# Kernel tuning notes

Measured on AMD Instinct MI355X. Metric: run time of the kernel, lower is better.

Reference implementation:

```python
import jax, jax.numpy as jnp
import numpy as np

DIM = 1024
HEADS = 16
HEAD_DIM = DIM // HEADS
HIDDEN = 4 * DIM
EPS = 1e-6


def _layer_norm(x, scale, bias):
    mu = jnp.mean(x, axis=-1, keepdims=True)
    var = jnp.mean(jnp.square(x - mu), axis=-1, keepdims=True)
    return (x - mu) * jax.lax.rsqrt(var + EPS) * scale + bias


def setup_inputs() -> dict:
    key = jax.random.key(0)
    ks = jax.random.split(key, 8)
    s = 0.02
    return {
        "x": jax.random.normal(ks[0], (8, 1024, DIM), dtype=jnp.float32),
        "w_qkv": jax.random.normal(ks[1], (DIM, 3 * DIM), dtype=jnp.float32) * s,
        "b_qkv": jnp.zeros((3 * DIM,), jnp.float32),
        "w_proj": jax.random.normal(ks[2], (DIM, DIM), dtype=jnp.float32) * s,
        "b_proj": jnp.zeros((DIM,), jnp.float32),
        "ln1_scale": jnp.ones((DIM,), jnp.float32),
        "ln1_bias": jnp.zeros((DIM,), jnp.float32),
        "ln2_scale": jnp.ones((DIM,), jnp.float32),
        "ln2_bias": jnp.zeros((DIM,), jnp.float32),
        "w_fc1": jax.random.normal(ks[3], (DIM, HIDDEN), dtype=jnp.float32) * s,
        "b_fc1": jnp.zeros((HIDDEN,), jnp.float32),
        "w_fc2": jax.random.normal(ks[4], (HIDDEN, DIM), dtype=jnp.float32) * s,
        "b_fc2": jnp.zeros((DIM,), jnp.float32),
    }


def reference(x, w_qkv, b_qkv, w_proj, b_proj, ln1_scale, ln1_bias,
              ln2_scale, ln2_bias, w_fc1, b_fc1, w_fc2, b_fc2):
    B, N, C = x.shape
    scale = HEAD_DIM ** -0.5

    # --- attention branch ---
    h = _layer_norm(x, ln1_scale, ln1_bias)
    qkv = h @ w_qkv + b_qkv                          # [B,N,3C]
    qkv = qkv.reshape(B, N, 3, HEADS, HEAD_DIM)
    qkv = jnp.transpose(qkv, (2, 0, 3, 1, 4))        # [3,B,H,N,D]
    q, k, v = qkv[0], qkv[1], qkv[2]
    attn = jnp.einsum("bhnd,bhmd->bhnm", q, k) * scale
    attn = jax.nn.softmax(attn, axis=-1)
    o = jnp.einsum("bhnm,bhmd->bhnd", attn, v)       # [B,H,N,D]
    o = jnp.transpose(o, (0, 2, 1, 3)).reshape(B, N, C)
    x = x + (o @ w_proj + b_proj)

    # --- mlp branch ---
    h = _layer_norm(x, ln2_scale, ln2_bias)
    h = jax.nn.gelu(h @ w_fc1 + b_fc1)               # tanh approx, matches flax default
    x = x + (h @ w_fc2 + b_fc2)
    return x
```

## Files before the change

### kernel.cpp

```cpp
#include <hip/hip_runtime.h>

typedef __attribute__((ext_vector_type(8))) short short8;
typedef __attribute__((ext_vector_type(4))) float f32x4;
typedef unsigned short ushort;
typedef unsigned int uint;

#define DIM 1024
#define NSEQ 1024
#define BATCH 8
#define HEADS 16
#define HD 64
#define HIDDEN 4096
#define NROWS (BATCH * NSEQ)

__device__ inline ushort f2bf(float f) {
  uint u = __float_as_uint(f);
  u += 0x7fff + ((u >> 16) & 1);
  return (ushort)(u >> 16);
}

__device__ inline f32x4 zero4() {
  f32x4 z; z[0] = 0.f; z[1] = 0.f; z[2] = 0.f; z[3] = 0.f; return z;
}

__device__ inline float gelu_fast(float x) {
  float u2 = 1.5957691216057308f * (x + 0.044715f * x * x * x);
  float e = __builtin_amdgcn_exp2f(-1.4426950408889634f * u2);
  return x / (1.0f + e);
}

#define GLDS16(g, l)                                                  \
  __builtin_amdgcn_global_load_lds(                                   \
      (const __attribute__((address_space(1))) void*)(g),             \
      (__attribute__((address_space(3))) void*)(l), 16, 0, 0)

#define WAITVM(n) asm volatile("s_waitcnt vmcnt(" #n ")" ::: "memory")

__global__ __launch_bounds__(256) void ln_kernel(
    const float* __restrict__ x, const float* __restrict__ sc,
    const float* __restrict__ bi, ushort* __restrict__ out) {
  int row = blockIdx.x;
  int t = threadIdx.x;
  const float4 v = reinterpret_cast<const float4*>(x + (size_t)row * DIM)[t];
  float s = v.x + v.y + v.z + v.w;
  float s2 = v.x * v.x + v.y * v.y + v.z * v.z + v.w * v.w;
#pragma unroll
  for (int off = 32; off >= 1; off >>= 1) {
    s += __shfl_xor(s, off);
    s2 += __shfl_xor(s2, off);
  }
  __shared__ float ps[4], ps2[4];
  int w = t >> 6;
  if ((t & 63) == 0) { ps[w] = s; ps2[w] = s2; }
  __syncthreads();
  s = ps[0] + ps[1] + ps[2] + ps[3];
  s2 = ps2[0] + ps2[1] + ps2[2] + ps2[3];
  float mu = s * (1.0f / DIM);
  float var = s2 * (1.0f / DIM) - mu * mu;
  float rstd = rsqrtf(var + 1e-6f);
  float4 scv = reinterpret_cast<const float4*>(sc)[t];
  float4 biv = reinterpret_cast<const float4*>(bi)[t];
  ushort4 o;
  o.x = f2bf((v.x - mu) * rstd * scv.x + biv.x);
  o.y = f2bf((v.y - mu) * rstd * scv.y + biv.y);
  o.z = f2bf((v.z - mu) * rstd * scv.z + biv.z);
  o.w = f2bf((v.w - mu) * rstd * scv.w + biv.w);
  reinterpret_cast<ushort4*>(out + (size_t)row * DIM)[t] = o;
}

__global__ __launch_bounds__(256) void wtrans_kernel(
    const float* __restrict__ w, ushort* __restrict__ wt, int K, int N) {
  __shared__ float tile[32][33];
  int n0 = blockIdx.x * 32, k0 = blockIdx.y * 32;
  int tx = threadIdx.x & 31, ty = threadIdx.x >> 5;
#pragma unroll
  for (int j = 0; j < 4; j++)
    tile[ty + 8 * j][tx] = w[(size_t)(k0 + ty + 8 * j) * N + n0 + tx];
  __syncthreads();
#pragma unroll
  for (int j = 0; j < 4; j++)
    wt[(size_t)(n0 + ty + 8 * j) * K + k0 + tx] = f2bf(tile[tx][ty + 8 * j]);
}

__global__ __launch_bounds__(256) void vtrans_kernel(
    const ushort* __restrict__ qkv, ushort* __restrict__ vT) {
  __shared__ ushort Ts[64 * 64];
  int bh = blockIdx.y;
  int b = bh >> 4, h = bh & 15;
  int n0 = blockIdx.x * 64;
  int t = threadIdx.x;
  const ushort* src = qkv + (size_t)b * NSEQ * 3072 + 2048 + h * 64;
#pragma unroll
  for (int i = 0; i < 2; i++) {
    int ci = i * 256 + t;
    int rr = ci >> 3, c = ci & 7;
    short8 v = *reinterpret_cast<const short8*>(src + (size_t)(n0 + rr) * 3072 + c * 8);
    *reinterpret_cast<short8*>(&Ts[rr * 64 + ((c ^ (rr >> 3)) & 7) * 8]) = v;
  }
  __syncthreads();
  ushort* dst = vT + (size_t)bh * 64 * NSEQ;
#pragma unroll
  for (int i = 0; i < 2; i++) {
    int ci = i * 256 + t;
    int dd = ci >> 3, c = ci & 7;
    short8 v;
#pragma unroll
    for (int j = 0; j < 8; j++) {
      int nn = c * 8 + j;
      v[j] = (short)Ts[nn * 64 + (((dd >> 3) ^ (nn >> 3)) & 7) * 8 + (dd & 7)];
    }
    *reinterpret_cast<short8*>(dst + (size_t)dd * NSEQ + n0 + c * 8) = v;
  }
}

template <int BN, int EPI>
__global__ __launch_bounds__(512, 2) void gemm256_kernel(
    const ushort* __restrict__ A, const ushort* __restrict__ Bt,
    const float* __restrict__ bias, const float* __restrict__ res,
    void* __restrict__ outp, int M, int N, int K) {
  constexpr int BM = 256, BK = 32;
  constexpr int WM = (BN == 256) ? 2 : 4;
  constexpr int WN = 8 / WM;
  constexpr int MR = (BM / WM) / 16;
  constexpr int NR = (BN / WN) / 16;
  constexpr int PH = MR / 4;
  constexpr int AR = 2;
  constexpr int BR = BN / 128;
  static_assert(BN == 256 || BN == 128, "");

  __shared__ ushort As[4][BM * BK];
  __shared__ ushort Bs[4][BN * BK];

  int t = threadIdx.x, lane = t & 63, w = t >> 6;
  int wr = w / WN, wc = w % WN;
  int r = lane & 15, g = lane >> 4;

  int nwg = gridDim.x * gridDim.y;
  int flat = blockIdx.y * gridDim.x + blockIdx.x;
  int swzf = (flat & 7) * (nwg >> 3) + (flat >> 3);
  int bx = swzf % gridDim.x, by = swzf / gridDim.x;
  int m0 = by * BM, n0 = bx * BN;

  const ushort* Ab = A + (size_t)m0 * K;
  const ushort* Bb = Bt + (size_t)n0 * K;

  int srow = t >> 2;
  int sgc8 = (((t & 3) ^ (srow & 3) ^ ((srow >> 2) & 3)) & 3) * 8;
  int swb = (w << 4) * BK;
  int sw = ((g ^ (r & 3) ^ ((r >> 2) & 3)) & 3) * 8;

  auto stageA = [&](int kt2) {
    ushort* as = &As[kt2 & 3][0];
    int ko = kt2 * BK;
#pragma unroll
    for (int p = 0; p < AR; p++)
      GLDS16(Ab + (size_t)(p * 128 + srow) * K + ko + sgc8,
             as + p * 128 * BK + swb);
  };
  auto stageB = [&](int kt2) {
    ushort* bs = &Bs[kt2 & 3][0];
    int ko = kt2 * BK;
#pragma unroll
    for (int p = 0; p < BR; p++)
      GLDS16(Bb + (size_t)(p * 128 + srow) * K + ko + sgc8,
             bs + p * 128 * BK + swb);
  };

  f32x4 acc[MR][NR];
#pragma unroll
  for (int mi = 0; mi < MR; mi++)
#pragma unroll
    for (int ni = 0; ni < NR; ni++) acc[mi][ni] = zero4();

  int nkt = K / BK;

  stageA(0); stageB(0);
  stageA(1); stageB(1);
  stageA(2); stageB(2);
  if constexpr (BN == 256) WAITVM(8); else WAITVM(6);
  __builtin_amdgcn_s_barrier();
  asm volatile("" ::: "memory");

  for (int kt = 0; kt < nkt; kt++) {
    const ushort* as = &As[kt & 3][0];
    const ushort* bs = &Bs[kt & 3][0];
    short8 b[NR];
#pragma unroll
    for (int ph = 0; ph < PH; ph++) {
      if (ph == 0) {
#pragma unroll
        for (int ni = 0; ni < NR; ni++)
          b[ni] = *reinterpret_cast<const short8*>(
              &bs[(wc * (BN / WN) + ni * 16 + r) * BK + sw]);
      }
      short8 a[4];
#pragma unroll
      for (int i = 0; i < 4; i++)
        a[i] = *reinterpret_cast<const short8*>(
            &as[(wr * (BM / WM) + (ph * 4 + i) * 16 + r) * BK + sw]);
      if (kt + 3 < nkt) {
        if constexpr (PH == 2) {
          if (ph == 0) stageA(kt + 3); else stageB(kt + 3);
        } else {
          stageA(kt + 3); stageB(kt + 3);
        }
      }
      if (ph == PH - 1) {
        if (kt + 3 < nkt) {
          if constexpr (BN == 256) WAITVM(8); else WAITVM(6);
        } else if (kt + 2 < nkt) {
          if constexpr (BN == 256) WAITVM(4); else WAITVM(3);
        } else if (kt + 1 < nkt) {
          WAITVM(0);
        }
      }
      __builtin_amdgcn_s_barrier();
      asm volatile("s_waitcnt lgkmcnt(0)" ::: "memory");
      __builtin_amdgcn_sched_barrier(0);
      __builtin_amdgcn_s_setprio(1);
#pragma unroll
      for (int i = 0; i < 4; i++)
#pragma unroll
        for (int ni = 0; ni < NR; ni++)
          acc[ph * 4 + i][ni] = __builtin_amdgcn_mfma_f32_16x16x32_bf16(
              a[i], b[ni], acc[ph * 4 + i][ni], 0, 0, 0);
      __builtin_amdgcn_s_setprio(0);
      __builtin_amdgcn_s_barrier();
      asm volatile("" ::: "memory");
    }
  }

  int rg = g * 4;
#pragma unroll
  for (int mi = 0; mi < MR; mi++) {
#pragma unroll
    for (int ni = 0; ni < NR; ni++) {
      int row = m0 + wr * (BM / WM) + mi * 16 + rg;
      int col = n0 + wc * (BN / WN) + ni * 16 + r;
      float bv = bias[col];
#pragma unroll
      for (int j = 0; j < 4; j++) {
        float v = acc[mi][ni][j] + bv;
        if (EPI == 1) v = gelu_fast(v);
        if (EPI == 2) {
          reinterpret_cast<float*>(outp)[(size_t)(row + j) * N + col] =
              v + res[(size_t)(row + j) * N + col];
        } else {
          reinterpret_cast<ushort*>(outp)[(size_t)(row + j) * N + col] = f2bf(v);
        }
      }
    }
  }
}

#define SM_SCALE_L2E 0.18033688f
#define SM_BIAS_L2E 11.54156036f
__global__ __launch_bounds__(256) void attn_kernel(
    const ushort* __restrict__ qkv, const ushort* __restrict__ vT,
    ushort* __restrict__ o) {
  __shared__ ushort Kt[64 * 72];
  __shared__ ushort Vt[64 * 72];
  __shared__ ushort Pl[4][16 * 72];
  int q0 = blockIdx.x * 64, h = blockIdx.y, b = blockIdx.z;
  int t = threadIdx.x, lane = t & 63, w = t >> 6;
  int r = lane & 15, g = lane >> 4;
  const ushort* base = qkv + (size_t)b * NSEQ * 3072 + h * 64;
  const ushort* vbase = vT + (size_t)(b * HEADS + h) * 64 * NSEQ;

  short8 qf[2];
  {
    const ushort* qrow = base + (size_t)(q0 + w * 16 + r) * 3072;
    qf[0] = *reinterpret_cast<const short8*>(qrow + g * 8);
    qf[1] = *reinterpret_cast<const short8*>(qrow + 32 + g * 8);
  }

  float l[4] = {0.f, 0.f, 0.f, 0.f};
  f32x4 oacc[4];
#pragma unroll
  for (int db = 0; db < 4; db++) oacc[db] = zero4();

  int srw = t >> 3, sc8 = (t & 7) * 8;
  for (int kt = 0; kt < NSEQ / 64; kt++) {
    int k0 = kt * 64;
    short8 kreg[2], vreg[2];
#pragma unroll
    for (int i = 0; i < 2; i++) {
      int rw = srw + i * 32;
      kreg[i] = *reinterpret_cast<const short8*>(base + 1024 + (size_t)(k0 + rw) * 3072 + sc8);
      vreg[i] = *reinterpret_cast<const short8*>(vbase + (size_t)rw * NSEQ + k0 + sc8);
    }
    __syncthreads();
#pragma unroll
    for (int i = 0; i < 2; i++) {
      int rw = srw + i * 32;
      *reinterpret_cast<short8*>(&Kt[rw * 72 + sc8]) = kreg[i];
      *reinterpret_cast<short8*>(&Vt[rw * 72 + sc8]) = vreg[i];
    }
    __syncthreads();

#pragma unroll
    for (int kb = 0; kb < 4; kb++) {
      short8 kf0 = *reinterpret_cast<const short8*>(&Kt[(kb * 16 + r) * 72 + g * 8]);
      short8 kf1 = *reinterpret_cast<const short8*>(&Kt[(kb * 16 + r) * 72 + 32 + g * 8]);
      f32x4 z = zero4();
      z = __builtin_amdgcn_mfma_f32_16x16x32_bf16(qf[0], kf0, z, 0, 0, 0);
      z = __builtin_amdgcn_mfma_f32_16x16x32_bf16(qf[1], kf1, z, 0, 0, 0);
#pragma unroll
      for (int j = 0; j < 4; j++) {
        float p = __builtin_amdgcn_exp2f(fmaf(z[j], SM_SCALE_L2E, -SM_BIAS_L2E));
        l[j] += p;
        Pl[w][(g * 4 + j) * 72 + kb * 16 + r] = (ushort)(__float_as_uint(p) >> 16);
      }
    }

#pragma unroll
    for (int ks = 0; ks < 2; ks++) {
      short8 pa = *reinterpret_cast<const short8*>(&Pl[w][r * 72 + ks * 32 + g * 8]);
#pragma unroll
      for (int db = 0; db < 4; db++) {
        short8 vb = *reinterpret_cast<const short8*>(&Vt[(db * 16 + r) * 72 + ks * 32 + g * 8]);
        oacc[db] = __builtin_amdgcn_mfma_f32_16x16x32_bf16(pa, vb, oacc[db], 0, 0, 0);
      }
    }
  }

#pragma unroll
  for (int j = 0; j < 4; j++) {
#pragma unroll
    for (int off = 8; off >= 1; off >>= 1) l[j] += __shfl_xor(l[j], off);
    l[j] = 1.0f / l[j];
  }

#pragma unroll
  for (int db = 0; db < 4; db++)
#pragma unroll
    for (int j = 0; j < 4; j++) {
      size_t row = (size_t)b * NSEQ + q0 + w * 16 + g * 4 + j;
      int col = h * 64 + db * 16 + r;
      o[row * DIM + col] = f2bf(oacc[db][j] * l[j]);
    }
}

extern "C" void kernel_launch(void* const* d_in, const int* in_sizes, int n_in,
                              void* d_out, int out_size, void* d_ws, size_t ws_size,
                              hipStream_t stream) {
  const float* x      = (const float*)d_in[0];
  const float* w_qkv  = (const float*)d_in[1];
  const float* b_qkv  = (const float*)d_in[2];
  const float* w_proj = (const float*)d_in[3];
  const float* b_proj = (const float*)d_in[4];
  const float* ln1s   = (const float*)d_in[5];
  const float* ln1b   = (const float*)d_in[6];
  const float* ln2s   = (const float*)d_in[7];
  const float* ln2b   = (const float*)d_in[8];
  const float* w_fc1  = (const float*)d_in[9];
  const float* b_fc1  = (const float*)d_in[10];
  const float* w_fc2  = (const float*)d_in[11];
  const float* b_fc2  = (const float*)d_in[12];
  float* out = (float*)d_out;

  char* ws = (char*)d_ws;
  ushort* wqkv_t  = (ushort*)(ws);
  ushort* wproj_t = (ushort*)(ws + 6291456);
  ushort* wfc1_t  = (ushort*)(ws + 8388608);
  ushort* wfc2_t  = (ushort*)(ws + 16777216);
  ushort* hbuf    = (ushort*)(ws + 25165824);
  float*  x1      = (float*)(ws + 41943040);
  ushort* vTb     = (ushort*)(ws + 41943040);
  ushort* qkv     = (ushort*)(ws + 75497472);
  ushort* obuf    = (ushort*)(ws + 125829120);
  ushort* fc1a    = qkv;

  wtrans_kernel<<<dim3(3072 / 32, 1024 / 32), 256, 0, stream>>>(w_qkv, wqkv_t, 1024, 3072);
  wtrans_kernel<<<dim3(1024 / 32, 1024 / 32), 256, 0, stream>>>(w_proj, wproj_t, 1024, 1024);
  wtrans_kernel<<<dim3(4096 / 32, 1024 / 32), 256, 0, stream>>>(w_fc1, wfc1_t, 1024, 4096);
  wtrans_kernel<<<dim3(1024 / 32, 4096 / 32), 256, 0, stream>>>(w_fc2, wfc2_t, 4096, 1024);

  ln_kernel<<<NROWS, 256, 0, stream>>>(x, ln1s, ln1b, hbuf);
  gemm256_kernel<128, 0><<<dim3(3072 / 128, NROWS / 256), 512, 0, stream>>>(
      hbuf, wqkv_t, b_qkv, nullptr, qkv, NROWS, 3072, 1024);
  vtrans_kernel<<<dim3(NSEQ / 64, BATCH * HEADS), 256, 0, stream>>>(qkv, vTb);
  attn_kernel<<<dim3(NSEQ / 64, HEADS, BATCH), 256, 0, stream>>>(qkv, vTb, obuf);
  gemm256_kernel<128, 2><<<dim3(1024 / 128, NROWS / 256), 512, 0, stream>>>(
      obuf, wproj_t, b_proj, x, x1, NROWS, 1024, 1024);

  ln_kernel<<<NROWS, 256, 0, stream>>>(x1, ln2s, ln2b, hbuf);
  gemm256_kernel<256, 1><<<dim3(4096 / 256, NROWS / 256), 512, 0, stream>>>(
      hbuf, wfc1_t, b_fc1, nullptr, fc1a, NROWS, 4096, 1024);
  gemm256_kernel<128, 2><<<dim3(1024 / 128, NROWS / 256), 512, 0, stream>>>(
      fc1a, wfc2_t, b_fc2, x1, out, NROWS, 1024, 4096);
}
```

Before: 398.8 us.

## Software-pipeline GEMM with register double-buffered fragments and one barrier per k-tile

Restructures the GEMM main loop so the LDS fragments for the next k-tile are loaded into a second register set while the MFMAs for the current tile run. A and B are staged together three tiles ahead, and there is now one barrier per k-tile instead of several per phase. K becomes a template constant so loop bounds and address strides are known at compile time. The aim is to hide LDS read latency and cut synchronisation overhead, at the cost of more VGPRs and a tighter dependence on ds_read completion ordering around the barrier.

```diff
diff --git a/kernel.cpp b/kernel.cpp
--- a/kernel.cpp
+++ b/kernel.cpp
@@ -35,6 +35,7 @@
       (__attribute__((address_space(3))) void*)(l), 16, 0, 0)
 
 #define WAITVM(n) asm volatile("s_waitcnt vmcnt(" #n ")" ::: "memory")
+#define SBAR() asm volatile("s_barrier" ::: "memory")
 
 __global__ __launch_bounds__(256) void ln_kernel(
     const float* __restrict__ x, const float* __restrict__ sc,
@@ -113,20 +114,21 @@
   }
 }
 
-template <int BN, int EPI>
+template <int BN, int EPI, int KK>
 __global__ __launch_bounds__(512, 2) void gemm256_kernel(
     const ushort* __restrict__ A, const ushort* __restrict__ Bt,
     const float* __restrict__ bias, const float* __restrict__ res,
-    void* __restrict__ outp, int M, int N, int K) {
+    void* __restrict__ outp, int M, int N) {
   constexpr int BM = 256, BK = 32;
   constexpr int WM = (BN == 256) ? 2 : 4;
   constexpr int WN = 8 / WM;
   constexpr int MR = (BM / WM) / 16;
   constexpr int NR = (BN / WN) / 16;
-  constexpr int PH = MR / 4;
   constexpr int AR = 2;
   constexpr int BR = BN / 128;
+  constexpr int nkt = KK / BK;
   static_assert(BN == 256 || BN == 128, "");
+  static_assert(nkt >= 4 && (nkt % 2) == 0, "");
 
   __shared__ ushort As[4][BM * BK];
   __shared__ ushort Bs[4][BN * BK];
@@ -141,93 +143,78 @@
   int bx = swzf % gridDim.x, by = swzf / gridDim.x;
   int m0 = by * BM, n0 = bx * BN;
 
-  const ushort* Ab = A + (size_t)m0 * K;
-  const ushort* Bb = Bt + (size_t)n0 * K;
+  const ushort* Ab = A + (size_t)m0 * KK;
+  const ushort* Bb = Bt + (size_t)n0 * KK;
 
   int srow = t >> 2;
   int sgc8 = (((t & 3) ^ (srow & 3) ^ ((srow >> 2) & 3)) & 3) * 8;
   int swb = (w << 4) * BK;
   int sw = ((g ^ (r & 3) ^ ((r >> 2) & 3)) & 3) * 8;
 
-  auto stageA = [&](int kt2) {
+  auto stageAB = [&](int kt2) {
     ushort* as = &As[kt2 & 3][0];
-    int ko = kt2 * BK;
-#pragma unroll
-    for (int p = 0; p < AR; p++)
-      GLDS16(Ab + (size_t)(p * 128 + srow) * K + ko + sgc8,
-             as + p * 128 * BK + swb);
-  };
-  auto stageB = [&](int kt2) {
     ushort* bs = &Bs[kt2 & 3][0];
     int ko = kt2 * BK;
 #pragma unroll
+    for (int p = 0; p < AR; p++)
+      GLDS16(Ab + (size_t)(p * 128 + srow) * KK + ko + sgc8,
+             as + p * 128 * BK + swb);
+#pragma unroll
     for (int p = 0; p < BR; p++)
-      GLDS16(Bb + (size_t)(p * 128 + srow) * K + ko + sgc8,
+      GLDS16(Bb + (size_t)(p * 128 + srow) * KK + ko + sgc8,
              bs + p * 128 * BK + swb);
   };
 
+  auto ldfrags = [&](int kt2, short8 (&fa_)[MR], short8 (&fb_)[NR]) {
+    const ushort* as = &As[kt2 & 3][0];
+    const ushort* bs = &Bs[kt2 & 3][0];
+#pragma unroll
+    for (int mi = 0; mi < MR; mi++)
+      fa_[mi] = *reinterpret_cast<const short8*>(
+          &as[(wr * (BM / WM) + mi * 16 + r) * BK + sw]);
+#pragma unroll
+    for (int ni = 0; ni < NR; ni++)
+      fb_[ni] = *reinterpret_cast<const short8*>(
+          &bs[(wc * (BN / WN) + ni * 16 + r) * BK + sw]);
+  };
+
   f32x4 acc[MR][NR];
 #pragma unroll
   for (int mi = 0; mi < MR; mi++)
 #pragma unroll
     for (int ni = 0; ni < NR; ni++) acc[mi][ni] = zero4();
 
-  int nkt = K / BK;
-
-  stageA(0); stageB(0);
-  stageA(1); stageB(1);
-  stageA(2); stageB(2);
-  if constexpr (BN == 256) WAITVM(8); else WAITVM(6);
-  __builtin_amdgcn_s_barrier();
-  asm volatile("" ::: "memory");
-
-  for (int kt = 0; kt < nkt; kt++) {
-    const ushort* as = &As[kt & 3][0];
-    const ushort* bs = &Bs[kt & 3][0];
-    short8 b[NR];
-#pragma unroll
-    for (int ph = 0; ph < PH; ph++) {
-      if (ph == 0) {
-#pragma unroll
-        for (int ni = 0; ni < NR; ni++)
-          b[ni] = *reinterpret_cast<const short8*>(
-              &bs[(wc * (BN / WN) + ni * 16 + r) * BK + sw]);
-      }
-      short8 a[4];
-#pragma unroll
-      for (int i = 0; i < 4; i++)
-        a[i] = *reinterpret_cast<const short8*>(
-            &as[(wr * (BM / WM) + (ph * 4 + i) * 16 + r) * BK + sw]);
-      if (kt + 3 < nkt) {
-        if constexpr (PH == 2) {
-          if (ph == 0) stageA(kt + 3); else stageB(kt + 3);
-        } else {
-          stageA(kt + 3); stageB(kt + 3);
-        }
-      }
-      if (ph == PH - 1) {
-        if (kt + 3 < nkt) {
-          if constexpr (BN == 256) WAITVM(8); else WAITVM(6);
-        } else if (kt + 2 < nkt) {
-          if constexpr (BN == 256) WAITVM(4); else WAITVM(3);
-        } else if (kt + 1 < nkt) {
-          WAITVM(0);
-        }
-      }
-      __builtin_amdgcn_s_barrier();
-      asm volatile("s_waitcnt lgkmcnt(0)" ::: "memory");
-      __builtin_amdgcn_sched_barrier(0);
-      __builtin_amdgcn_s_setprio(1);
-#pragma unroll
-      for (int i = 0; i < 4; i++)
-#pragma unroll
-        for (int ni = 0; ni < NR; ni++)
-          acc[ph * 4 + i][ni] = __builtin_amdgcn_mfma_f32_16x16x32_bf16(
-              a[i], b[ni], acc[ph * 4 + i][ni], 0, 0, 0);
-      __builtin_amdgcn_s_setprio(0);
-      __builtin_amdgcn_s_barrier();
-      asm volatile("" ::: "memory");
-    }
+  auto body = [&](int kt, short8 (&ca)[MR], short8 (&cb)[NR],
+                  short8 (&na)[MR], short8 (&nb)[NR]) {
+    if (kt + 1 < nkt) ldfrags(kt + 1, na, nb);
+    if (kt + 3 < nkt) stageAB(kt + 3);
+    __builtin_amdgcn_s_setprio(1);
+#pragma unroll
+    for (int mi = 0; mi < MR; mi++)
+#pragma unroll
+      for (int ni = 0; ni < NR; ni++)
+        acc[mi][ni] = __builtin_amdgcn_mfma_f32_16x16x32_bf16(
+            ca[mi], cb[ni], acc[mi][ni], 0, 0, 0);
+    __builtin_amdgcn_s_setprio(0);
+    if (kt + 3 < nkt) {
+      if constexpr (BN == 256) WAITVM(4); else WAITVM(3);
+      SBAR();
+    } else if (kt + 2 < nkt) {
+      WAITVM(0);
+      SBAR();
+    }
+  };
+
+  stageAB(0); stageAB(1); stageAB(2);
+  if constexpr (BN == 256) WAITVM(4); else WAITVM(3);
+  SBAR();
+
+  short8 fa[2][MR], fb[2][NR];
+  ldfrags(0, fa[0], fb[0]);
+#pragma unroll 1
+  for (int k2 = 0; k2 < nkt / 2; k2++) {
+    body(2 * k2 + 0, fa[0], fb[0], fa[1], fb[1]);
+    body(2 * k2 + 1, fa[1], fb[1], fa[0], fb[0]);
   }
 
   int rg = g * 4;
@@ -377,16 +364,16 @@
   wtrans_kernel<<<dim3(1024 / 32, 4096 / 32), 256, 0, stream>>>(w_fc2, wfc2_t, 4096, 1024);
 
   ln_kernel<<<NROWS, 256, 0, stream>>>(x, ln1s, ln1b, hbuf);
-  gemm256_kernel<128, 0><<<dim3(3072 / 128, NROWS / 256), 512, 0, stream>>>(
-      hbuf, wqkv_t, b_qkv, nullptr, qkv, NROWS, 3072, 1024);
+  gemm256_kernel<128, 0, 1024><<<dim3(3072 / 128, NROWS / 256), 512, 0, stream>>>(
+      hbuf, wqkv_t, b_qkv, nullptr, qkv, NROWS, 3072);
   vtrans_kernel<<<dim3(NSEQ / 64, BATCH * HEADS), 256, 0, stream>>>(qkv, vTb);
   attn_kernel<<<dim3(NSEQ / 64, HEADS, BATCH), 256, 0, stream>>>(qkv, vTb, obuf);
-  gemm256_kernel<128, 2><<<dim3(1024 / 128, NROWS / 256), 512, 0, stream>>>(
-      obuf, wproj_t, b_proj, x, x1, NROWS, 1024, 1024);
+  gemm256_kernel<128, 2, 1024><<<dim3(1024 / 128, NROWS / 256), 512, 0, stream>>>(
+      obuf, wproj_t, b_proj, x, x1, NROWS, 1024);
 
   ln_kernel<<<NROWS, 256, 0, stream>>>(x1, ln2s, ln2b, hbuf);
-  gemm256_kernel<256, 1><<<dim3(4096 / 256, NROWS / 256), 512, 0, stream>>>(
-      hbuf, wfc1_t, b_fc1, nullptr, fc1a, NROWS, 4096, 1024);
-  gemm256_kernel<128, 2><<<dim3(1024 / 128, NROWS / 256), 512, 0, stream>>>(
-      fc1a, wfc2_t, b_fc2, x1, out, NROWS, 1024, 4096);
-}
+  gemm256_kernel<256, 1, 1024><<<dim3(4096 / 256, NROWS / 256), 512, 0, stream>>>(
+      hbuf, wfc1_t, b_fc1, nullptr, fc1a, NROWS, 4096);
+  gemm256_kernel<128, 2, 4096><<<dim3(1024 / 128, NROWS / 256), 512, 0, stream>>>(
+      fc1a, wfc2_t, b_fc2, x1, out, NROWS, 1024);
+}
```

Result: faster. 389.7 us (-2.3%).
